# Performance work log

Measured on AMD Instinct MI355X. Metric: run time of the kernel, lower is better.

## Reference

```python
import jax, jax.numpy as jnp
import numpy as np

H = 8  # num_heads (init kwarg)

def setup_inputs() -> dict:
    key = jax.random.key(0)
    k1, k2, k3 = jax.random.split(key, 3)
    B, N, C = 1, 256, 512
    x = jax.random.normal(k1, (B, N, C), dtype=jnp.float32)
    W_att = jax.random.normal(k2, (C, 5 * C), dtype=jnp.float32) * 0.02
    b_att = jnp.zeros((5 * C,), dtype=jnp.float32)
    W_out = jax.random.normal(k3, (C, C), dtype=jnp.float32) * 0.02
    b_out = jnp.zeros((C,), dtype=jnp.float32)
    return {"x": x, "W_att": W_att, "b_att": b_att, "W_out": W_out, "b_out": b_out}

def reference(x, W_att, b_att, W_out, b_out):
    B, N, C = x.shape
    D = C // H
    scale = D ** -0.5
    # att_proj: [B,N,5C] -> rearrange 'b n (h d)' with h=H -> [B,H,N,5D] -> chunk 5
    p = (x @ W_att + b_att).reshape(B, N, H, 5 * D).transpose(0, 2, 1, 3)
    q, kj, kk, vj, vk = jnp.split(p, 5, axis=-1)  # each [B,H,N,D]
    # third-order scores: [B,H,N,N,N]
    scores = jnp.einsum('bhid,bhjd,bhkd->bhijk', q, kj, kk) * scale
    # softmax over flattened (j,k) per query i
    w = jax.nn.softmax(scores.reshape(B, H, N, N * N), axis=-1).reshape(B, H, N, N, N)
    y = jnp.einsum('bhijk,bhjd,bhkd->bhid', w, vj, vk)  # [B,H,N,D]
    y = y.transpose(0, 2, 1, 3).reshape(B, N, C)  # 'b h n d -> b n (h d)'
    return y @ W_out + b_out
```

## Files before the change

### kernel.cpp

```cpp
#include <hip/hip_runtime.h>
#include <stdint.h>


typedef __attribute__((ext_vector_type(4))) float f32x4;
typedef __attribute__((ext_vector_type(4))) short s16x4;
typedef __attribute__((ext_vector_type(8))) short s16x8;

#define H_ 8
#define N_ 256
#define D_ 64
#define C_ 512
#define NC5 2560
#define SCALE_LOG2E 0.1803368801111204f

__device__ __forceinline__ unsigned short f2bf_rne(float x) {
  union { float f; unsigned u; } a; a.f = x;
  unsigned r = a.u + 0x7fffu + ((a.u >> 16) & 1u);
  return (unsigned short)(r >> 16);
}

__device__ __forceinline__ unsigned pk_bf16(float a, float b) {
#if __has_builtin(__builtin_amdgcn_cvt_pk_bf16_f32)
  typedef __attribute__((ext_vector_type(2))) __bf16 bf16x2;
  union { bf16x2 v; unsigned u; } u;
  u.v = __builtin_amdgcn_cvt_pk_bf16_f32(a, b);
  return u.u;
#else
  return (unsigned)f2bf_rne(a) | ((unsigned)f2bf_rne(b) << 16);
#endif
}

__device__ __forceinline__ f32x4 mfma32(s16x8 a, s16x8 b, f32x4 c) {
  return __builtin_amdgcn_mfma_f32_16x16x32_bf16(a, b, c, 0, 0, 0);
}

__device__ __forceinline__ f32x4 mfma16(s16x4 a, s16x4 b, f32x4 c) {
#if __has_builtin(__builtin_amdgcn_mfma_f32_16x16x16bf16_1k)
  return __builtin_amdgcn_mfma_f32_16x16x16bf16_1k(a, b, c, 0, 0, 0);
#else
  asm volatile("s_nop 1\n\t"
               "v_mfma_f32_16x16x16_bf16 %0, %1, %2, %0\n\t"
               "s_nop 7\n\t"
               "s_nop 2"
               : "+v"(c) : "v"(a), "v"(b));
  return c;
#endif
}

__global__ __launch_bounds__(256) void proj_kernel(
    const float* __restrict__ x, const float* __restrict__ W,
    const float* __restrict__ b,
    float* __restrict__ qS, float* __restrict__ kj,
    unsigned short* __restrict__ kkB, float* __restrict__ vj,
    float* __restrict__ vkT) {
  __shared__ float As[32][17];
  __shared__ float Bs[32][68];
  const int bx = blockIdx.x;
  const int by = blockIdx.y;
  const int tid = threadIdx.x;
  const int m = tid >> 4;
  const int c4 = (tid & 15) * 4;
  float acc0 = 0.f, acc1 = 0.f, acc2 = 0.f, acc3 = 0.f;

  const int lk = tid & 31;
  const int lm = tid >> 5;
  const int bk = tid >> 4;

  for (int k0 = 0; k0 < C_; k0 += 32) {
    As[lk][lm] = x[(by * 16 + lm) * C_ + k0 + lk];
    As[lk][lm + 8] = x[(by * 16 + lm + 8) * C_ + k0 + lk];
    *(f32x4*)&Bs[bk][c4] = *(const f32x4*)&W[(k0 + bk) * NC5 + bx * 64 + c4];
    *(f32x4*)&Bs[bk + 16][c4] =
        *(const f32x4*)&W[(k0 + bk + 16) * NC5 + bx * 64 + c4];
    __syncthreads();
#pragma unroll
    for (int kq = 0; kq < 32; ++kq) {
      float a = As[kq][m];
      f32x4 bv = *(const f32x4*)&Bs[kq][c4];
      acc0 += a * bv.x; acc1 += a * bv.y; acc2 += a * bv.z; acc3 += a * bv.w;
    }
    __syncthreads();
  }

  const int i = by * 16 + m;
  const int col0 = bx * 64 + c4;
  const int h = (bx * 64) / 320;
  const int part = ((bx * 64) % 320) >> 6;
  const int d0 = c4;
  float v0 = acc0 + b[col0 + 0];
  float v1 = acc1 + b[col0 + 1];
  float v2 = acc2 + b[col0 + 2];
  float v3 = acc3 + b[col0 + 3];
  const int idx = (h * N_ + i) * D_ + d0;
  if (part == 0) {
    f32x4 o = {v0 * SCALE_LOG2E, v1 * SCALE_LOG2E, v2 * SCALE_LOG2E,
               v3 * SCALE_LOG2E};
    *(f32x4*)(qS + idx) = o;
  } else if (part == 1) {
    f32x4 o = {v0, v1, v2, v3};
    *(f32x4*)(kj + idx) = o;
  } else if (part == 2) {
    union { unsigned u[2]; s16x4 v4; } t;
    t.u[0] = pk_bf16(v0, v1);
    t.u[1] = pk_bf16(v2, v3);
    *(s16x4*)(kkB + idx) = t.v4;
  } else if (part == 3) {
    f32x4 o = {v0, v1, v2, v3};
    *(f32x4*)(vj + idx) = o;
  } else {
    vkT[(h * D_ + d0 + 0) * N_ + i] = v0;
    vkT[(h * D_ + d0 + 1) * N_ + i] = v1;
    vkT[(h * D_ + d0 + 2) * N_ + i] = v2;
    vkT[(h * D_ + d0 + 3) * N_ + i] = v3;
  }
}

__global__ __launch_bounds__(256, 2) void flash3_kernel(
    const float* __restrict__ qS,
    const float* __restrict__ kjF,
    const unsigned short* __restrict__ kkB,
    const float* __restrict__ vjF,
    const float* __restrict__ vkT,
    float* __restrict__ slab,
    float* __restrict__ lslab) {
  const int h = blockIdx.x;
  const int ic = blockIdx.y;
  const int jc = blockIdx.z;
  const int wave = threadIdx.x >> 6;
  const int lane = threadIdx.x & 63;
  const int q = lane >> 4;
  const int c = lane & 15;
  const int i0 = ic * 64;

  const float* qh = qS + h * (N_ * D_);
  const float* kjh = kjF + h * (N_ * D_);
  const unsigned short* kkh = kkB + h * (N_ * D_);
  const float* vjh = vjF + h * (N_ * D_);
  const float* vkh = vkT + h * (D_ * N_);

  f32x4 acc[4][4];
#pragma unroll
  for (int mb = 0; mb < 4; ++mb)
#pragma unroll
    for (int nb = 0; nb < 4; ++nb) acc[mb][nb] = (f32x4){0.f, 0.f, 0.f, 0.f};
  float lac[4] = {0.f, 0.f, 0.f, 0.f};

  for (int jj = 0; jj < 2; ++jj) {
    const int j = jc * 8 + wave * 2 + jj;
    const f32x4 kj0a = *(const f32x4*)(kjh + j * D_ + q * 8);
    const f32x4 kj0b = *(const f32x4*)(kjh + j * D_ + q * 8 + 4);
    const f32x4 kj1a = *(const f32x4*)(kjh + j * D_ + 32 + q * 8);
    const f32x4 kj1b = *(const f32x4*)(kjh + j * D_ + 32 + q * 8 + 4);
    float vjv[4];
#pragma unroll
    for (int mb = 0; mb < 4; ++mb) vjv[mb] = vjh[j * D_ + mb * 16 + c];

    s16x8 qf[4][2];
#pragma unroll
    for (int nb = 0; nb < 4; ++nb) {
      const float* qp = qh + (i0 + nb * 16 + c) * D_;
      f32x4 a0 = *(const f32x4*)(qp + q * 8);
      f32x4 a1 = *(const f32x4*)(qp + q * 8 + 4);
      f32x4 b0 = *(const f32x4*)(qp + 32 + q * 8);
      f32x4 b1 = *(const f32x4*)(qp + 32 + q * 8 + 4);
      union { unsigned u[4]; s16x8 v; } t0, t1;
      t0.u[0] = pk_bf16(a0.x * kj0a.x, a0.y * kj0a.y);
      t0.u[1] = pk_bf16(a0.z * kj0a.z, a0.w * kj0a.w);
      t0.u[2] = pk_bf16(a1.x * kj0b.x, a1.y * kj0b.y);
      t0.u[3] = pk_bf16(a1.z * kj0b.z, a1.w * kj0b.w);
      t1.u[0] = pk_bf16(b0.x * kj1a.x, b0.y * kj1a.y);
      t1.u[1] = pk_bf16(b0.z * kj1a.z, b0.w * kj1a.w);
      t1.u[2] = pk_bf16(b1.x * kj1b.x, b1.y * kj1b.y);
      t1.u[3] = pk_bf16(b1.z * kj1b.z, b1.w * kj1b.w);
      qf[nb][0] = t0.v;
      qf[nb][1] = t1.v;
    }

    for (int k0 = 0; k0 < N_; k0 += 64) {
#pragma unroll
      for (int mb = 0; mb < 4; ++mb) {
        const unsigned short* kp = kkh + (k0 + mb * 16 + c) * D_;
        s16x8 ka0 = *(const s16x8*)(kp + q * 8);
        s16x8 ka1 = *(const s16x8*)(kp + 32 + q * 8);
        f32x4 fv[4];
#pragma unroll
        for (int md = 0; md < 4; ++md)
          fv[md] =
              *(const f32x4*)(vkh + (md * 16 + c) * N_ + k0 + mb * 16 + q * 4);

        f32x4 st[4];
#pragma unroll
        for (int nb = 0; nb < 4; ++nb) {
          f32x4 z = (f32x4){0.f, 0.f, 0.f, 0.f};
          z = mfma32(ka0, qf[nb][0], z);
          z = mfma32(ka1, qf[nb][1], z);
          st[nb] = z;
        }
        s16x4 pn[4];
#pragma unroll
        for (int nb = 0; nb < 4; ++nb) {
          float p0 = __builtin_exp2f(st[nb].x);
          float p1 = __builtin_exp2f(st[nb].y);
          float p2 = __builtin_exp2f(st[nb].z);
          float p3 = __builtin_exp2f(st[nb].w);
          lac[nb] += (p0 + p1) + (p2 + p3);
          union { unsigned u[2]; s16x4 v4; } t;
          t.u[0] = pk_bf16(p0, p1);
          t.u[1] = pk_bf16(p2, p3);
          pn[nb] = t.v4;
        }
#pragma unroll
        for (int md = 0; md < 4; ++md) {
          float s = vjv[md];
          union { unsigned u[2]; s16x4 v4; } t;
          t.u[0] = pk_bf16(fv[md].x * s, fv[md].y * s);
          t.u[1] = pk_bf16(fv[md].z * s, fv[md].w * s);
#pragma unroll
          for (int nb = 0; nb < 4; ++nb)
            acc[md][nb] = mfma16(t.v4, pn[nb], acc[md][nb]);
        }
      }
    }
  }

  __shared__ float red[2][64 * 68];
  __shared__ float lredA[2][64];
  __shared__ float lredB[64];

  float lv[4];
#pragma unroll
  for (int nb = 0; nb < 4; ++nb) {
    float v = lac[nb];
    v += __shfl_xor(v, 16);
    v += __shfl_xor(v, 32);
    lv[nb] = v;
  }

  if (wave >= 2) {
    float* dst = red[wave - 2];
#pragma unroll
    for (int mb = 0; mb < 4; ++mb)
#pragma unroll
      for (int nb = 0; nb < 4; ++nb)
        *(f32x4*)&dst[(nb * 16 + c) * 68 + mb * 16 + q * 4] = acc[mb][nb];
    if (q == 0)
#pragma unroll
      for (int nb = 0; nb < 4; ++nb) lredA[wave - 2][nb * 16 + c] = lv[nb];
  }
  __syncthreads();
  if (wave < 2) {
    const float* src = red[wave];
#pragma unroll
    for (int mb = 0; mb < 4; ++mb)
#pragma unroll
      for (int nb = 0; nb < 4; ++nb)
        acc[mb][nb] += *(const f32x4*)&src[(nb * 16 + c) * 68 + mb * 16 + q * 4];
    if (q == 0)
#pragma unroll
      for (int nb = 0; nb < 4; ++nb) lv[nb] += lredA[wave][nb * 16 + c];
  }
  __syncthreads();
  if (wave == 1) {
#pragma unroll
    for (int mb = 0; mb < 4; ++mb)
#pragma unroll
      for (int nb = 0; nb < 4; ++nb)
        *(f32x4*)&red[0][(nb * 16 + c) * 68 + mb * 16 + q * 4] = acc[mb][nb];
    if (q == 0)
#pragma unroll
      for (int nb = 0; nb < 4; ++nb) lredB[nb * 16 + c] = lv[nb];
  }
  __syncthreads();
  if (wave == 0) {
    float* out = slab + ((h * 32 + jc) * 4 + ic) * 4096;
#pragma unroll
    for (int mb = 0; mb < 4; ++mb)
#pragma unroll
      for (int nb = 0; nb < 4; ++nb) {
        f32x4 v = acc[mb][nb] +
                  *(const f32x4*)&red[0][(nb * 16 + c) * 68 + mb * 16 + q * 4];
        *(f32x4*)(out + (nb * 16 + c) * 64 + mb * 16 + q * 4) = v;
      }
    if (q == 0)
#pragma unroll
      for (int nb = 0; nb < 4; ++nb)
        lslab[(h * 32 + jc) * 256 + ic * 64 + nb * 16 + c] =
            lv[nb] + lredB[nb * 16 + c];
  }
}

__global__ __launch_bounds__(256) void reduce_kernel(
    const float* __restrict__ slab, const float* __restrict__ lslab,
    float* __restrict__ yn) {
  int idx = blockIdx.x * 256 + threadIdx.x;
  int h = idx >> 14;
  int r = idx & 16383;
  int ic = r >> 12;
  int il = (r >> 6) & 63;
  int d = r & 63;
  float s = 0.f, l = 0.f;
#pragma unroll 4
  for (int jc = 0; jc < 32; ++jc) {
    s += slab[(((h * 32 + jc) * 4 + ic) << 12) + il * 64 + d];
    l += lslab[(h * 32 + jc) * 256 + ic * 64 + il];
  }
  int i = ic * 64 + il;
  yn[i * C_ + h * 64 + d] = s / l;
}

__global__ __launch_bounds__(256) void out_gemm(
    const float* __restrict__ A, const float* __restrict__ W,
    const float* __restrict__ b, float* __restrict__ out) {
  __shared__ float As[32][17];
  __shared__ float Bs[32][68];
  const int bx = blockIdx.x;
  const int by = blockIdx.y;
  const int tid = threadIdx.x;
  const int m = tid >> 4;
  const int c4 = (tid & 15) * 4;
  float acc0 = 0.f, acc1 = 0.f, acc2 = 0.f, acc3 = 0.f;

  const int lk = tid & 31;
  const int lm = tid >> 5;
  const int bk = tid >> 4;

  for (int k0 = 0; k0 < C_; k0 += 32) {
    As[lk][lm] = A[(by * 16 + lm) * C_ + k0 + lk];
    As[lk][lm + 8] = A[(by * 16 + lm + 8) * C_ + k0 + lk];
    *(f32x4*)&Bs[bk][c4] = *(const f32x4*)&W[(k0 + bk) * C_ + bx * 64 + c4];
    *(f32x4*)&Bs[bk + 16][c4] =
        *(const f32x4*)&W[(k0 + bk + 16) * C_ + bx * 64 + c4];
    __syncthreads();
#pragma unroll
    for (int kq = 0; kq < 32; ++kq) {
      float a = As[kq][m];
      f32x4 bv = *(const f32x4*)&Bs[kq][c4];
      acc0 += a * bv.x; acc1 += a * bv.y; acc2 += a * bv.z; acc3 += a * bv.w;
    }
    __syncthreads();
  }

  const int i = by * 16 + m;
  const int col = bx * 64 + c4;
  f32x4 o = {acc0 + b[col + 0], acc1 + b[col + 1], acc2 + b[col + 2],
             acc3 + b[col + 3]};
  *(f32x4*)(out + i * C_ + col) = o;
}

extern "C" void kernel_launch(void* const* d_in, const int* in_sizes, int n_in,
                              void* d_out, int out_size, void* d_ws,
                              size_t ws_size, hipStream_t stream) {
  const float* x     = (const float*)d_in[0];
  const float* W_att = (const float*)d_in[1];
  const float* b_att = (const float*)d_in[2];
  const float* W_out = (const float*)d_in[3];
  const float* b_out = (const float*)d_in[4];

  char* ws = (char*)d_ws;
  float* slab           = (float*)(ws + 0);
  float* lslab          = (float*)(ws + 16777216);
  float* qSb            = (float*)(ws + 17039360);
  float* kj             = (float*)(ws + 17563648);
  unsigned short* kkB   = (unsigned short*)(ws + 18087936);
  float* vj             = (float*)(ws + 18350080);
  float* vkT            = (float*)(ws + 18874368);
  float* yn             = (float*)(ws + 19398656);

  proj_kernel<<<dim3(40, 16), 256, 0, stream>>>(x, W_att, b_att, qSb, kj, kkB,
                                                vj, vkT);
  flash3_kernel<<<dim3(8, 4, 32), 256, 0, stream>>>(qSb, kj, kkB, vj, vkT,
                                                    slab, lslab);
  reduce_kernel<<<dim3(512), 256, 0, stream>>>(slab, lslab, yn);
  out_gemm<<<dim3(8, 16), 256, 0, stream>>>(yn, W_out, b_out, (float*)d_out);
}
```

Baseline: 228.6 us.

## Factor vj scaling out of inner loop and store vk as bf16

Changes the projection kernel to write vk transposed as bf16, so the attention kernel loads MFMA operands directly with no per-iteration conversion. The vj multiply is factored out of the k loop: each j's accumulator is scaled by vj once at the end and added into a shared-memory tile with LDS atomics, which replaces the multi-stage cross-wave reduction. The launch bound is raised to 3 blocks per CU. The trade-offs are many LDS float atomics, the added rounding from bf16 vk, and register pressure from the per-j accumulators under the tighter occupancy bound.

```diff
diff --git a/kernel.cpp b/kernel.cpp
--- a/kernel.cpp
+++ b/kernel.cpp
@@ -52,7 +52,7 @@
     const float* __restrict__ b,
     float* __restrict__ qS, float* __restrict__ kj,
     unsigned short* __restrict__ kkB, float* __restrict__ vj,
-    float* __restrict__ vkT) {
+    unsigned short* __restrict__ vkBT) {
   __shared__ float As[32][17];
   __shared__ float Bs[32][68];
   const int bx = blockIdx.x;
@@ -108,21 +108,24 @@
     f32x4 o = {v0, v1, v2, v3};
     *(f32x4*)(vj + idx) = o;
   } else {
-    vkT[(h * D_ + d0 + 0) * N_ + i] = v0;
-    vkT[(h * D_ + d0 + 1) * N_ + i] = v1;
-    vkT[(h * D_ + d0 + 2) * N_ + i] = v2;
-    vkT[(h * D_ + d0 + 3) * N_ + i] = v3;
-  }
-}
-
-__global__ __launch_bounds__(256, 2) void flash3_kernel(
+    vkBT[(h * D_ + d0 + 0) * N_ + i] = f2bf_rne(v0);
+    vkBT[(h * D_ + d0 + 1) * N_ + i] = f2bf_rne(v1);
+    vkBT[(h * D_ + d0 + 2) * N_ + i] = f2bf_rne(v2);
+    vkBT[(h * D_ + d0 + 3) * N_ + i] = f2bf_rne(v3);
+  }
+}
+
+__global__ __launch_bounds__(256, 3) void flash3_kernel(
     const float* __restrict__ qS,
     const float* __restrict__ kjF,
     const unsigned short* __restrict__ kkB,
     const float* __restrict__ vjF,
-    const float* __restrict__ vkT,
+    const unsigned short* __restrict__ vkBT,
     float* __restrict__ slab,
     float* __restrict__ lslab) {
+  __shared__ float Yl[64 * 68];
+  __shared__ float ll[64];
+
   const int h = blockIdx.x;
   const int ic = blockIdx.y;
   const int jc = blockIdx.z;
@@ -132,29 +135,25 @@
   const int c = lane & 15;
   const int i0 = ic * 64;
 
+  for (int t = threadIdx.x; t < 64 * 68; t += 256) Yl[t] = 0.f;
+  if (threadIdx.x < 64) ll[threadIdx.x] = 0.f;
+  __syncthreads();
+
   const float* qh = qS + h * (N_ * D_);
   const float* kjh = kjF + h * (N_ * D_);
   const unsigned short* kkh = kkB + h * (N_ * D_);
   const float* vjh = vjF + h * (N_ * D_);
-  const float* vkh = vkT + h * (D_ * N_);
-
-  f32x4 acc[4][4];
-#pragma unroll
-  for (int mb = 0; mb < 4; ++mb)
-#pragma unroll
-    for (int nb = 0; nb < 4; ++nb) acc[mb][nb] = (f32x4){0.f, 0.f, 0.f, 0.f};
+  const unsigned short* vkh = vkBT + h * (D_ * N_);
+
   float lac[4] = {0.f, 0.f, 0.f, 0.f};
 
   for (int jj = 0; jj < 2; ++jj) {
     const int j = jc * 8 + wave * 2 + jj;
+
     const f32x4 kj0a = *(const f32x4*)(kjh + j * D_ + q * 8);
     const f32x4 kj0b = *(const f32x4*)(kjh + j * D_ + q * 8 + 4);
     const f32x4 kj1a = *(const f32x4*)(kjh + j * D_ + 32 + q * 8);
     const f32x4 kj1b = *(const f32x4*)(kjh + j * D_ + 32 + q * 8 + 4);
-    float vjv[4];
-#pragma unroll
-    for (int mb = 0; mb < 4; ++mb) vjv[mb] = vjh[j * D_ + mb * 16 + c];
-
     s16x8 qf[4][2];
 #pragma unroll
     for (int nb = 0; nb < 4; ++nb) {
@@ -176,17 +175,23 @@
       qf[nb][1] = t1.v;
     }
 
+    f32x4 acc[4][4];
+#pragma unroll
+    for (int md = 0; md < 4; ++md)
+#pragma unroll
+      for (int nb = 0; nb < 4; ++nb) acc[md][nb] = (f32x4){0.f, 0.f, 0.f, 0.f};
+
     for (int k0 = 0; k0 < N_; k0 += 64) {
 #pragma unroll
       for (int mb = 0; mb < 4; ++mb) {
         const unsigned short* kp = kkh + (k0 + mb * 16 + c) * D_;
         s16x8 ka0 = *(const s16x8*)(kp + q * 8);
         s16x8 ka1 = *(const s16x8*)(kp + 32 + q * 8);
-        f32x4 fv[4];
+        s16x4 av[4];
 #pragma unroll
         for (int md = 0; md < 4; ++md)
-          fv[md] =
-              *(const f32x4*)(vkh + (md * 16 + c) * N_ + k0 + mb * 16 + q * 4);
+          av[md] = *(const s16x4*)(vkh + (md * 16 + c) * N_ + k0 + mb * 16 +
+                                   q * 4);
 
         f32x4 st[4];
 #pragma unroll
@@ -210,82 +215,46 @@
           pn[nb] = t.v4;
         }
 #pragma unroll
-        for (int md = 0; md < 4; ++md) {
-          float s = vjv[md];
-          union { unsigned u[2]; s16x4 v4; } t;
-          t.u[0] = pk_bf16(fv[md].x * s, fv[md].y * s);
-          t.u[1] = pk_bf16(fv[md].z * s, fv[md].w * s);
+        for (int md = 0; md < 4; ++md)
 #pragma unroll
           for (int nb = 0; nb < 4; ++nb)
-            acc[md][nb] = mfma16(t.v4, pn[nb], acc[md][nb]);
-        }
+            acc[md][nb] = mfma16(av[md], pn[nb], acc[md][nb]);
       }
     }
-  }
-
-  __shared__ float red[2][64 * 68];
-  __shared__ float lredA[2][64];
-  __shared__ float lredB[64];
-
-  float lv[4];
+
+#pragma unroll
+    for (int md = 0; md < 4; ++md) {
+      f32x4 vs = *(const f32x4*)(vjh + j * D_ + md * 16 + q * 4);
+#pragma unroll
+      for (int nb = 0; nb < 4; ++nb) {
+        float* p = &Yl[(nb * 16 + c) * 68 + md * 16 + q * 4];
+        atomicAdd(p + 0, acc[md][nb].x * vs.x);
+        atomicAdd(p + 1, acc[md][nb].y * vs.y);
+        atomicAdd(p + 2, acc[md][nb].z * vs.z);
+        atomicAdd(p + 3, acc[md][nb].w * vs.w);
+      }
+    }
+  }
+
 #pragma unroll
   for (int nb = 0; nb < 4; ++nb) {
     float v = lac[nb];
     v += __shfl_xor(v, 16);
     v += __shfl_xor(v, 32);
-    lv[nb] = v;
-  }
-
-  if (wave >= 2) {
-    float* dst = red[wave - 2];
-#pragma unroll
-    for (int mb = 0; mb < 4; ++mb)
-#pragma unroll
-      for (int nb = 0; nb < 4; ++nb)
-        *(f32x4*)&dst[(nb * 16 + c) * 68 + mb * 16 + q * 4] = acc[mb][nb];
-    if (q == 0)
-#pragma unroll
-      for (int nb = 0; nb < 4; ++nb) lredA[wave - 2][nb * 16 + c] = lv[nb];
+    if (q == 0) atomicAdd(&ll[nb * 16 + c], v);
   }
   __syncthreads();
-  if (wave < 2) {
-    const float* src = red[wave];
-#pragma unroll
-    for (int mb = 0; mb < 4; ++mb)
-#pragma unroll
-      for (int nb = 0; nb < 4; ++nb)
-        acc[mb][nb] += *(const f32x4*)&src[(nb * 16 + c) * 68 + mb * 16 + q * 4];
-    if (q == 0)
-#pragma unroll
-      for (int nb = 0; nb < 4; ++nb) lv[nb] += lredA[wave][nb * 16 + c];
-  }
-  __syncthreads();
-  if (wave == 1) {
-#pragma unroll
-    for (int mb = 0; mb < 4; ++mb)
-#pragma unroll
-      for (int nb = 0; nb < 4; ++nb)
-        *(f32x4*)&red[0][(nb * 16 + c) * 68 + mb * 16 + q * 4] = acc[mb][nb];
-    if (q == 0)
-#pragma unroll
-      for (int nb = 0; nb < 4; ++nb) lredB[nb * 16 + c] = lv[nb];
-  }
-  __syncthreads();
-  if (wave == 0) {
+
+  {
     float* out = slab + ((h * 32 + jc) * 4 + ic) * 4096;
-#pragma unroll
-    for (int mb = 0; mb < 4; ++mb)
-#pragma unroll
-      for (int nb = 0; nb < 4; ++nb) {
-        f32x4 v = acc[mb][nb] +
-                  *(const f32x4*)&red[0][(nb * 16 + c) * 68 + mb * 16 + q * 4];
-        *(f32x4*)(out + (nb * 16 + c) * 64 + mb * 16 + q * 4) = v;
-      }
-    if (q == 0)
-#pragma unroll
-      for (int nb = 0; nb < 4; ++nb)
-        lslab[(h * 32 + jc) * 256 + ic * 64 + nb * 16 + c] =
-            lv[nb] + lredB[nb * 16 + c];
+    const int row = threadIdx.x >> 2;
+    const int col0 = (threadIdx.x & 3) * 16;
+#pragma unroll
+    for (int u = 0; u < 4; ++u)
+      *(f32x4*)(out + row * 64 + col0 + u * 4) =
+          *(const f32x4*)&Yl[row * 68 + col0 + u * 4];
+    if (threadIdx.x < 64)
+      lslab[(h * 32 + jc) * 256 + ic * 64 + threadIdx.x] = ll[threadIdx.x];
   }
 }
 
@@ -363,12 +332,12 @@
   float* kj             = (float*)(ws + 17563648);
   unsigned short* kkB   = (unsigned short*)(ws + 18087936);
   float* vj             = (float*)(ws + 18350080);
-  float* vkT            = (float*)(ws + 18874368);
+  unsigned short* vkBT  = (unsigned short*)(ws + 18874368);
   float* yn             = (float*)(ws + 19398656);
 
   proj_kernel<<<dim3(40, 16), 256, 0, stream>>>(x, W_att, b_att, qSb, kj, kkB,
-                                                vj, vkT);
-  flash3_kernel<<<dim3(8, 4, 32), 256, 0, stream>>>(qSb, kj, kkB, vj, vkT,
+                                                vj, vkBT);
+  flash3_kernel<<<dim3(8, 4, 32), 256, 0, stream>>>(qSb, kj, kkB, vj, vkBT,
                                                     slab, lslab);
   reduce_kernel<<<dim3(512), 256, 0, stream>>>(slab, lslab, yn);
   out_gemm<<<dim3(8, 16), 256, 0, stream>>>(yn, W_out, b_out, (float*)d_out);
```

After: 450.5 us. 97.1% more time.
